# Optimization experiments

Measured on AMD Instinct MI355X. Metric: run time of the kernel, lower is better.

The kernel has to match this reference:

```python
import jax, jax.numpy as jnp
import numpy as np

# Dims: N=batch, C=heads (depthwise channels), H=W=seq_len (square causal map)
N, C, H, W = 2, 16, 2048, 2048
R, S = 6, 11            # kernel: R over out rows (queries), S over cols (keys)
PAD_H, PAD_W = 5, 5     # pad_h = R-1 (causal in h), pad_w = (S-1)//2 (centered in w)


def setup_inputs() -> dict:
    key = jax.random.key(0)
    k1, k2 = jax.random.split(key)
    x = jax.random.normal(k1, (N, C, H, W), dtype=jnp.float32)
    weight = jax.random.normal(k2, (C, R, S), dtype=jnp.float32) * 0.1
    return {"x": x, "weight": weight}


def reference(x, weight):
    # Causal (lower-triangular) mask h >= w, as in the Triton kernels'
    # `in_h >= in_w` / `out_h >= out_w` masking.
    causal_mask = jnp.tril(jnp.ones((H, W), dtype=bool))  # [H, W]

    # Mask input causally (matches bwd_weight masking x with in_h >= in_w).
    xm = jnp.where(causal_mask, x, jnp.zeros((), x.dtype))  # [N,C,H,W]

    # Depthwise cross-correlation:
    #   y[b,c,p,q] = sum_{r,s} w[c,r,s] * xm[b,c, p+r-PAD_H, q+s-PAD_W]
    # Asymmetric padding keeps output HxW: (PAD_H, R-1-PAD_H) in h => causal
    # taps p-(R-1)..p; (PAD_W, S-1-PAD_W) in w => centered taps.
    y = jax.lax.conv_general_dilated(
        xm,
        weight[:, None, :, :],  # [C,1,R,S] OIHW, depthwise via groups=C
        window_strides=(1, 1),
        padding=((PAD_H, R - 1 - PAD_H), (PAD_W, S - 1 - PAD_W)),
        dimension_numbers=("NCHW", "OIHW", "NCHW"),
        feature_group_count=C,
    )

    # Mask output causally (matches bwd_input masking dout with out_h >= out_w).
    return jnp.where(causal_mask, y, jnp.zeros((), y.dtype))
```

## Files before the change

kernel.cpp:

```cpp
#include <hip/hip_runtime.h>
#include <stdint.h>


#define HDIM 2048
#define WDIM 2048
#define CH   16

#define PITCH 80
#define XROWS 69
#define NSL   (XROWS * 20)

typedef float    f32x4 __attribute__((ext_vector_type(4)));
typedef __fp16   h16x2 __attribute__((ext_vector_type(2)));
typedef _Float16 f16x8 __attribute__((ext_vector_type(8)));

__global__ __launch_bounds__(256, 6)
void dwconv_mfma(const float* __restrict__ x, const float* __restrict__ wgt,
                 float* __restrict__ out) {
  const int bx = blockIdx.x, by = blockIdx.y, zp = blockIdx.z;
  const int q0 = bx * 64, p0 = by * 64;
  const int tid = threadIdx.x;
  const size_t pb0 = (size_t)zp * HDIM * WDIM;
  const size_t pb1 = (size_t)(zp + CH) * HDIM * WDIM;

  if (by < bx) {
    const float4 z = make_float4(0.f, 0.f, 0.f, 0.f);
    float* o0 = out + pb0 + (size_t)p0 * WDIM + q0;
    float* o1 = out + pb1 + (size_t)p0 * WDIM + q0;
#pragma unroll
    for (int i = 0; i < 4; ++i) {
      int idx = i * 256 + tid;
      int row = idx >> 4, c4 = idx & 15;
      *(float4*)(o0 + (size_t)row * WDIM + 4 * c4) = z;
      *(float4*)(o1 + (size_t)row * WDIM + 4 * c4) = z;
    }
    return;
  }

  __shared__ __attribute__((aligned(16))) _Float16 sx[2][XROWS * PITCH];

  const bool pure = (bx >= 1) && (bx <= 30) && (by >= bx + 2);

  auto stage_plane = [&](const float* __restrict__ xpl,
                         _Float16* __restrict__ buf) {
#pragma unroll
    for (int j = 0; j < 6; ++j) {
      int slot = j * 256 + tid;
      if (slot < NSL) {
        int row = slot / 20;
        int c4 = slot - row * 20;
        int ih = p0 - 5 + row;
        int cb = q0 - 8 + 4 * c4;
        float4 v = make_float4(0.f, 0.f, 0.f, 0.f);
        if (pure) {
          v = *(const float4*)(xpl + (size_t)ih * WDIM + cb);
        } else if (ih >= 0) {
          bool fullv = (cb >= 0) && (cb + 3 <= ih) && (cb + 3 < WDIM);
          if (fullv) {
            v = *(const float4*)(xpl + (size_t)ih * WDIM + cb);
          } else {
            float* vv = &v.x;
#pragma unroll
            for (int e = 0; e < 4; ++e) {
              int iw = cb + e;
              if (iw >= 0 && iw < WDIM && iw <= ih)
                vv[e] = xpl[(size_t)ih * WDIM + iw];
            }
          }
        }
        union { h16x2 h[2]; uint2 u; } cv;
        cv.h[0] = __builtin_amdgcn_cvt_pkrtz(v.x, v.y);
        cv.h[1] = __builtin_amdgcn_cvt_pkrtz(v.z, v.w);
        *(uint2*)&buf[row * PITCH + 4 * c4] = cv.u;
      }
    }
  };

  stage_plane(x + pb0, &sx[0][0]);
  stage_plane(x + pb1, &sx[1][0]);

  const int lane = tid & 63;
  const int j16 = lane & 15;
  const int wk  = lane >> 4;
  const int wid = tid >> 6;
  const float* __restrict__ wcp = wgt + zp * 66;
  f16x8 aw[6];
#pragma unroll
  for (int r = 0; r < 6; ++r) {
#pragma unroll
    for (int i = 0; i < 8; ++i) {
      int d = 8 * wk + i - j16 - 3;
      aw[r][i] = (_Float16)((d >= 0 && d <= 10) ? wcp[r * 11 + d] : 0.f);
    }
  }

  __syncthreads();

  const bool dmask = (by == bx);

#pragma unroll 1
  for (int pl = 0; pl < 2; ++pl) {
    const _Float16* __restrict__ lb = &sx[pl][0];
    float* __restrict__ op = out + (pl ? pb1 : pb0);

    f32x4 acc[4];
#pragma unroll
    for (int qt = 0; qt < 4; ++qt) acc[qt] = (f32x4){0.f, 0.f, 0.f, 0.f};

#pragma unroll
    for (int qt = 0; qt < 4; ++qt) {
#pragma unroll
      for (int r = 0; r < 6; ++r) {
        int off = (16 * wid + j16 + r) * PITCH + 16 * qt + 8 * wk;
        f16x8 xb = *(const f16x8*)&lb[off];
        acc[qt] =
            __builtin_amdgcn_mfma_f32_16x16x32_f16(aw[r], xb, acc[qt], 0, 0, 0);
      }
    }

    const int p = p0 + 16 * wid + j16;
#pragma unroll
    for (int qt = 0; qt < 4; ++qt) {
      const int q = q0 + 16 * qt + 4 * wk;
      f32x4 a = acc[qt];
      if (dmask) {
#pragma unroll
        for (int reg = 0; reg < 4; ++reg)
          if (q + reg > p) a[reg] = 0.f;
      }
      *(float4*)(op + (size_t)p * WDIM + q) =
          make_float4(a[0], a[1], a[2], a[3]);
    }
  }
}

extern "C" void kernel_launch(void* const* d_in, const int* in_sizes, int n_in,
                              void* d_out, int out_size, void* d_ws, size_t ws_size,
                              hipStream_t stream) {
  const float* x   = (const float*)d_in[0];
  const float* wgt = (const float*)d_in[1];
  float* out       = (float*)d_out;
  dim3 grid(WDIM / 64, HDIM / 64, CH);
  dwconv_mfma<<<grid, dim3(256), 0, stream>>>(x, wgt, out);
}
```

Measured before the change: 334.3 us.

## Split upper-triangle zeroing into separate kernel and persist over lower tiles

Splits the work into two kernels. A separate kernel zeros the strictly-upper part of each output row with coalesced stores. The conv kernel becomes persistent: it loops over only the lower-triangular 64x64 tiles of all 32 planes, handles one plane per tile and recovers tile coordinates from a triangular index. This removes the blocks launched only to write zeros and evens out load balance, but adds a second launch, per-tile sqrt index decoding and extra barriers per iteration. It also drops the two-plane reuse of weights and staging, and limits LDS to one plane.

```diff
diff --git a/kernel.cpp b/kernel.cpp
--- a/kernel.cpp
+++ b/kernel.cpp
@@ -5,44 +5,72 @@
 #define HDIM 2048
 #define WDIM 2048
 #define CH   16
-
+#define NPLANE 32
 #define PITCH 80
 #define XROWS 69
 #define NSL   (XROWS * 20)
+#define NTILES 528
+#define TOTTILES (NPLANE * NTILES)
+#define NBLK 2048
 
 typedef float    f32x4 __attribute__((ext_vector_type(4)));
 typedef __fp16   h16x2 __attribute__((ext_vector_type(2)));
 typedef _Float16 f16x8 __attribute__((ext_vector_type(8)));
 
-__global__ __launch_bounds__(256, 6)
-void dwconv_mfma(const float* __restrict__ x, const float* __restrict__ wgt,
-                 float* __restrict__ out) {
-  const int bx = blockIdx.x, by = blockIdx.y, zp = blockIdx.z;
-  const int q0 = bx * 64, p0 = by * 64;
+__global__ __launch_bounds__(256, 8)
+void zero_upper(float* __restrict__ out) {
+  const int gw = ((blockIdx.x << 8) + threadIdx.x) >> 6;
+  const int lane = threadIdx.x & 63;
+  const float4 z = make_float4(0.f, 0.f, 0.f, 0.f);
+  for (int r = gw; r < NPLANE * HDIM; r += 4096) {
+    const int p = r & (HDIM - 1);
+    float* row = out + ((size_t)r << 11);
+    int c0 = p + 1;
+    if (c0 >= WDIM) continue;
+    int a0 = (c0 + 3) & ~3;
+    int head = a0 - c0;
+    if (head > WDIM - c0) head = WDIM - c0;
+    if (lane < head) row[c0 + lane] = 0.f;
+    for (int c = a0 + 4 * lane; c < WDIM; c += 256)
+      *(float4*)(row + c) = z;
+  }
+}
+
+__global__ __launch_bounds__(256, 8)
+void dwconv_tiles(const float* __restrict__ x, const float* __restrict__ wgt,
+                  float* __restrict__ out) {
+  __shared__ __attribute__((aligned(16))) _Float16 sx[XROWS * PITCH];
   const int tid = threadIdx.x;
-  const size_t pb0 = (size_t)zp * HDIM * WDIM;
-  const size_t pb1 = (size_t)(zp + CH) * HDIM * WDIM;
+  const int lane = tid & 63;
+  const int j16 = lane & 15;
+  const int wk  = lane >> 4;
+  const int wid = tid >> 6;
 
-  if (by < bx) {
-    const float4 z = make_float4(0.f, 0.f, 0.f, 0.f);
-    float* o0 = out + pb0 + (size_t)p0 * WDIM + q0;
-    float* o1 = out + pb1 + (size_t)p0 * WDIM + q0;
+#pragma unroll 1
+  for (int f = blockIdx.x; f < TOTTILES; f += NBLK) {
+    const int plane = f / NTILES;
+    const int k = f - plane * NTILES;
+    int by = (int)((sqrtf(8.f * k + 1.f) - 1.f) * 0.5f);
+    while ((by + 1) * (by + 2) / 2 <= k) ++by;
+    while (by * (by + 1) / 2 > k) --by;
+    const int bx = k - by * (by + 1) / 2;
+    const int p0 = by << 6, q0 = bx << 6;
+    const size_t pb = (size_t)plane * ((size_t)HDIM * WDIM);
+    const float* __restrict__ xp = x + pb;
+    float* __restrict__ op = out + pb;
+
+    const float* __restrict__ wcp = wgt + (plane & (CH - 1)) * 66;
+    f16x8 aw[6];
 #pragma unroll
-    for (int i = 0; i < 4; ++i) {
-      int idx = i * 256 + tid;
-      int row = idx >> 4, c4 = idx & 15;
-      *(float4*)(o0 + (size_t)row * WDIM + 4 * c4) = z;
-      *(float4*)(o1 + (size_t)row * WDIM + 4 * c4) = z;
+    for (int r = 0; r < 6; ++r) {
+#pragma unroll
+      for (int i = 0; i < 8; ++i) {
+        int d = 8 * wk + i - j16 - 3;
+        aw[r][i] = (_Float16)((d >= 0 && d <= 10) ? wcp[r * 11 + d] : 0.f);
+      }
     }
-    return;
-  }
 
-  __shared__ __attribute__((aligned(16))) _Float16 sx[2][XROWS * PITCH];
-
-  const bool pure = (bx >= 1) && (bx <= 30) && (by >= bx + 2);
-
-  auto stage_plane = [&](const float* __restrict__ xpl,
-                         _Float16* __restrict__ buf) {
+    const bool pure = (bx >= 1) && (by >= bx + 2);
 #pragma unroll
     for (int j = 0; j < 6; ++j) {
       int slot = j * 256 + tid;
@@ -53,72 +81,46 @@
         int cb = q0 - 8 + 4 * c4;
         float4 v = make_float4(0.f, 0.f, 0.f, 0.f);
         if (pure) {
-          v = *(const float4*)(xpl + (size_t)ih * WDIM + cb);
+          v = *(const float4*)(xp + (size_t)ih * WDIM + cb);
         } else if (ih >= 0) {
           bool fullv = (cb >= 0) && (cb + 3 <= ih) && (cb + 3 < WDIM);
           if (fullv) {
-            v = *(const float4*)(xpl + (size_t)ih * WDIM + cb);
+            v = *(const float4*)(xp + (size_t)ih * WDIM + cb);
           } else {
             float* vv = &v.x;
 #pragma unroll
             for (int e = 0; e < 4; ++e) {
               int iw = cb + e;
               if (iw >= 0 && iw < WDIM && iw <= ih)
-                vv[e] = xpl[(size_t)ih * WDIM + iw];
+                vv[e] = xp[(size_t)ih * WDIM + iw];
             }
           }
         }
         union { h16x2 h[2]; uint2 u; } cv;
         cv.h[0] = __builtin_amdgcn_cvt_pkrtz(v.x, v.y);
         cv.h[1] = __builtin_amdgcn_cvt_pkrtz(v.z, v.w);
-        *(uint2*)&buf[row * PITCH + 4 * c4] = cv.u;
+        *(uint2*)&sx[row * PITCH + 4 * c4] = cv.u;
       }
     }
-  };
 
-  stage_plane(x + pb0, &sx[0][0]);
-  stage_plane(x + pb1, &sx[1][0]);
-
-  const int lane = tid & 63;
-  const int j16 = lane & 15;
-  const int wk  = lane >> 4;
-  const int wid = tid >> 6;
-  const float* __restrict__ wcp = wgt + zp * 66;
-  f16x8 aw[6];
-#pragma unroll
-  for (int r = 0; r < 6; ++r) {
-#pragma unroll
-    for (int i = 0; i < 8; ++i) {
-      int d = 8 * wk + i - j16 - 3;
-      aw[r][i] = (_Float16)((d >= 0 && d <= 10) ? wcp[r * 11 + d] : 0.f);
-    }
-  }
-
-  __syncthreads();
-
-  const bool dmask = (by == bx);
-
-#pragma unroll 1
-  for (int pl = 0; pl < 2; ++pl) {
-    const _Float16* __restrict__ lb = &sx[pl][0];
-    float* __restrict__ op = out + (pl ? pb1 : pb0);
+    __syncthreads();
 
     f32x4 acc[4];
 #pragma unroll
     for (int qt = 0; qt < 4; ++qt) acc[qt] = (f32x4){0.f, 0.f, 0.f, 0.f};
-
 #pragma unroll
     for (int qt = 0; qt < 4; ++qt) {
 #pragma unroll
       for (int r = 0; r < 6; ++r) {
         int off = (16 * wid + j16 + r) * PITCH + 16 * qt + 8 * wk;
-        f16x8 xb = *(const f16x8*)&lb[off];
+        f16x8 xb = *(const f16x8*)&sx[off];
         acc[qt] =
             __builtin_amdgcn_mfma_f32_16x16x32_f16(aw[r], xb, acc[qt], 0, 0, 0);
       }
     }
 
     const int p = p0 + 16 * wid + j16;
+    const bool dmask = (by == bx);
 #pragma unroll
     for (int qt = 0; qt < 4; ++qt) {
       const int q = q0 + 16 * qt + 4 * wk;
@@ -131,6 +133,8 @@
       *(float4*)(op + (size_t)p * WDIM + q) =
           make_float4(a[0], a[1], a[2], a[3]);
     }
+
+    __syncthreads();
   }
 }
 
@@ -140,6 +144,6 @@
   const float* x   = (const float*)d_in[0];
   const float* wgt = (const float*)d_in[1];
   float* out       = (float*)d_out;
-  dim3 grid(WDIM / 64, HDIM / 64, CH);
-  dwconv_mfma<<<grid, dim3(256), 0, stream>>>(x, wgt, out);
+  zero_upper<<<dim3(1024), dim3(256), 0, stream>>>(out);
+  dwconv_tiles<<<dim3(NBLK), dim3(256), 0, stream>>>(x, wgt, out);
 }
```

After: 414.8 us. +24.0%, slower.
